# Performance work log

Measured on AMD Instinct MI355X. Metric: run time of the kernel, lower is better.

## Reference

```python
import jax, jax.numpy as jnp
import numpy as np

B, N, NFEAT, NHID, NOUT = 16, 2048, 128, 128, 64
BN_EPS = 1e-5
LRELU_ALPHA = 0.2


def setup_inputs() -> dict:
    key = jax.random.key(0)
    ks = jax.random.split(key, 6)
    stdv = 1.0 / np.sqrt(NHID)
    return {
        "x": jax.random.normal(ks[0], (B, N, NFEAT), dtype=jnp.float32),
        "adj": jnp.zeros((N, N), dtype=jnp.float32),  # passed to GAT but unused
        "adj_gcn": jax.random.uniform(ks[1], (N, N), dtype=jnp.float32),
        "gcn_weight": jax.random.uniform(ks[2], (NFEAT, NHID), minval=-stdv, maxval=stdv, dtype=jnp.float32),
        "gcn_bias": jax.random.uniform(ks[3], (NHID,), minval=-stdv, maxval=stdv, dtype=jnp.float32),
        "bn_gamma": jnp.ones((NHID,), dtype=jnp.float32),
        "bn_beta": jnp.zeros((NHID,), dtype=jnp.float32),
        "gat_W": jax.random.normal(ks[4], (NFEAT, NOUT), dtype=jnp.float32) * 0.05,
    }


def reference(x, adj, adj_gcn, gcn_weight, gcn_bias, bn_gamma, bn_beta, gat_W):
    # --- GCN layer: adj @ (x @ W) + b ---
    support = jnp.einsum("bnc,cd->bnd", x, gcn_weight)
    h = jnp.einsum("nm,bmd->bnd", adj_gcn, support) + gcn_bias  # [B,N,nhid]
    # --- BatchNorm1d (training mode: batch stats over B,N per channel) ---
    mean = h.mean(axis=(0, 1))
    var = h.var(axis=(0, 1))
    h = (h - mean) * jax.lax.rsqrt(var + BN_EPS) * bn_gamma + bn_beta
    # --- ReLU ---
    h = jax.nn.relu(h)
    # --- GAT layer (adj arg unused, as in original) ---
    h_prime = jnp.einsum("bnd,de->bne", h, gat_W)  # [B,N,nout]
    e = jnp.einsum("bne,bme->bnm", h_prime, h_prime)  # [B,N,N]
    e = jnp.where(e > 0, e, LRELU_ALPHA * e)  # LeakyReLU(0.2)
    attention = jax.nn.softmax(e, axis=1)  # softmax over dim=1 (as in source)
    # repeat-mul-sum over dim=2 reduces exactly to row-sum scaling of h_prime
    out = h_prime * attention.sum(axis=2, keepdims=True)  # [B,N,nout]
    return out
```

## Files before the change

### kernel.cpp

```cpp
#include <hip/hip_runtime.h>
#include <math.h>

#define NB 16
#define NN 2048
#define NF 128
#define NH 128
#define NO 64

typedef short bf16x8 __attribute__((ext_vector_type(8)));
typedef float f32x4 __attribute__((ext_vector_type(4)));
typedef unsigned short u16;
typedef unsigned int u32;

#define LOG2E 1.4426950408889634f
#define EXPSHIFT 43.28085122666891f

__device__ __forceinline__ u16 f2bf(float f) {
  u32 u = __builtin_bit_cast(u32, f);
  return (u16)((u + 0x7fffu + ((u >> 16) & 1u)) >> 16);
}
__device__ __forceinline__ float bf2f(u16 h) {
  u32 u = ((u32)h) << 16;
  return __builtin_bit_cast(float, u);
}

__device__ __forceinline__ void gload16(const void* g, void* l) {
  __builtin_amdgcn_global_load_lds((const __attribute__((address_space(1))) void*)g,
                                   (__attribute__((address_space(3))) void*)l, 16, 0, 0);
}
__device__ __forceinline__ f32x4 mfma16(bf16x8 a, bf16x8 b, f32x4 c) {
  return __builtin_amdgcn_mfma_f32_16x16x32_bf16(a, b, c, 0, 0, 0);
}
__device__ __forceinline__ float explr(float z) {
  return __builtin_amdgcn_exp2f(fmaf(fmaxf(z, 0.2f * z), LOG2E, -EXPSHIFT));
}

__global__ __launch_bounds__(256) void k_prep(const float* __restrict__ x,
                                              const float* __restrict__ adj,
                                              const float* __restrict__ gcn_w,
                                              const float* __restrict__ gat_w,
                                              u16* __restrict__ suppT_sw,
                                              u16* __restrict__ adj_sw,
                                              u16* __restrict__ Wg_sw) {
  __shared__ __align__(16) u16 ts[64 * 136];
  __shared__ __align__(16) u16 Bs[16384];
  const int t = threadIdx.x;
  const int bid = blockIdx.x;
  if (bid == 0) {
#pragma unroll
    for (int it = 0; it < 4; ++it) {
      const int s = t + it * 256;
      const int kb = s >> 6, col = s & 63;
      u16 tmp[8];
#pragma unroll
      for (int j = 0; j < 8; ++j) tmp[j] = f2bf(gat_w[(kb * 8 + j) * 64 + col]);
      uint4 o;
      o.x = (u32)tmp[0] | ((u32)tmp[1] << 16);
      o.y = (u32)tmp[2] | ((u32)tmp[3] << 16);
      o.z = (u32)tmp[4] | ((u32)tmp[5] << 16);
      o.w = (u32)tmp[6] | ((u32)tmp[7] << 16);
      *(uint4*)&Wg_sw[(size_t)s * 8] = o;
    }
  } else if (bid < 1025) {
    const int tile = bid - 1;
    const int n0 = (tile >> 5) * 64, m0 = (tile & 31) * 64;
#pragma unroll
    for (int k = 0; k < 4; ++k) {
      const int s = t + k * 256;
      const int row = s >> 4, c4 = (s & 15) * 4;
      const float4 f = *(const float4*)&adj[(size_t)(n0 + row) * 2048 + m0 + c4];
      uint2 pk;
      pk.x = (u32)f2bf(f.x) | ((u32)f2bf(f.y) << 16);
      pk.y = (u32)f2bf(f.z) | ((u32)f2bf(f.w) << 16);
      *(uint2*)&ts[row * 136 + c4] = pk;
    }
    __syncthreads();
#pragma unroll
    for (int k = 0; k < 2; ++k) {
      const int s = t + k * 256;
      const int kb = s >> 6, row = s & 63;
      const uint4 v = *(const uint4*)&ts[row * 136 + kb * 8];
      *(uint4*)&adj_sw[(size_t)tile * 4096 + (size_t)s * 8] = v;
    }
  } else {
    const int sb = bid - 1025;
    const int m0g = sb * 64;
    const int w = t >> 6, l = t & 63;
    const int lg = l >> 4, lr = l & 15;
#pragma unroll
    for (int i = 0; i < 8; ++i) {
      const int s = t + i * 256;
      const int kb = s >> 7, d = s & 127;
      u16 tmp[8];
#pragma unroll
      for (int j = 0; j < 8; ++j) tmp[j] = f2bf(gcn_w[(kb * 8 + j) * 128 + d]);
      uint4 o;
      o.x = (u32)tmp[0] | ((u32)tmp[1] << 16);
      o.y = (u32)tmp[2] | ((u32)tmp[3] << 16);
      o.z = (u32)tmp[4] | ((u32)tmp[5] << 16);
      o.w = (u32)tmp[6] | ((u32)tmp[7] << 16);
      *(uint4*)&Bs[(size_t)s * 8] = o;
    }
#pragma unroll
    for (int k = 0; k < 8; ++k) {
      const int s = t + k * 256;
      const int row = s >> 5, c4 = (s & 31) * 4;
      const float4 f = *(const float4*)&x[(size_t)(m0g + row) * 128 + c4];
      uint2 pk;
      pk.x = (u32)f2bf(f.x) | ((u32)f2bf(f.y) << 16);
      pk.y = (u32)f2bf(f.z) | ((u32)f2bf(f.w) << 16);
      *(uint2*)&ts[row * 136 + c4] = pk;
    }
    __syncthreads();
    f32x4 acc[8];
#pragma unroll
    for (int nf = 0; nf < 8; ++nf) {
      acc[nf][0] = 0.f; acc[nf][1] = 0.f;
      acc[nf][2] = 0.f; acc[nf][3] = 0.f;
    }
#pragma unroll
    for (int ks = 0; ks < 4; ++ks) {
      const int kb = ks * 4 + lg;
      const bf16x8 a = *(const bf16x8*)&ts[(w * 16 + lr) * 136 + kb * 8];
#pragma unroll
      for (int nf = 0; nf < 8; ++nf) {
        const bf16x8 bb = *(const bf16x8*)&Bs[((size_t)kb * 128 + nf * 16 + lr) * 8];
        acc[nf] = mfma16(a, bb, acc[nf]);
      }
    }
    __syncthreads();
    u16* os = Bs;
#pragma unroll
    for (int nf = 0; nf < 8; ++nf) {
      const int d = nf * 16 + lr;
      const int mb = w * 16 + lg * 4;
      const u32 p0 = (u32)f2bf(acc[nf][0]) | ((u32)f2bf(acc[nf][1]) << 16);
      const u32 p1 = (u32)f2bf(acc[nf][2]) | ((u32)f2bf(acc[nf][3]) << 16);
      *(u32*)&os[d * 72 + mb] = p0;
      *(u32*)&os[d * 72 + mb + 2] = p1;
    }
    __syncthreads();
    const int b = m0g >> 11, mt = (m0g & 2047) >> 6;
#pragma unroll
    for (int i = 0; i < 4; ++i) {
      const int s = i * 256 + t;
      const int kb = s >> 7, d = s & 127;
      const uint4 v = *(const uint4*)&os[d * 72 + kb * 8];
      *(uint4*)&suppT_sw[((size_t)((b * 32 + mt) * 8 + kb)) * 1024 + (size_t)d * 8] = v;
    }
  }
}

__global__ __launch_bounds__(512) void k_gcn(const u16* __restrict__ adj_sw,
                                             const u16* __restrict__ suppT_sw,
                                             const float* __restrict__ bias,
                                             float* __restrict__ h,
                                             float* __restrict__ psum,
                                             float* __restrict__ psq) {
  const int flat = blockIdx.y * 32 + blockIdx.x;
  const int nf2 = (flat & 7) * 64 + (flat >> 3);
  const int b = nf2 >> 5, nt = nf2 & 31;
  const int n0 = nt * 64;
  const int t = threadIdx.x;
  const int w = t >> 6, l = t & 63;
  const int wm = w >> 1, wn = w & 1;
  const int lg = l >> 4, lr = l & 15;
  __shared__ __align__(16) u16 As[2][4096];
  __shared__ __align__(16) u16 Bs[2][8192];
  __shared__ float redS[4][128], redQ[4][128];

  f32x4 acc[4];
#pragma unroll
  for (int nf = 0; nf < 4; ++nf) {
    acc[nf][0] = 0.f; acc[nf][1] = 0.f;
    acc[nf][2] = 0.f; acc[nf][3] = 0.f;
  }

#define GCN_STAGE(buf, kt)                                                        \
  {                                                                               \
    gload16(adj_sw + ((size_t)(nt * 32 + (kt))) * 4096 + (size_t)t * 8,           \
            &As[buf][t * 8]);                                                     \
    _Pragma("unroll") for (int i = 0; i < 2; ++i) {                               \
      const int s = i * 512 + t;                                                  \
      gload16(suppT_sw + ((size_t)(b * 32 + (kt))) * 8192 + (size_t)s * 8,        \
              &Bs[buf][s * 8]);                                                   \
    }                                                                             \
  }

  GCN_STAGE(0, 0);
  __syncthreads();
  for (int kt = 0; kt < 32; ++kt) {
    const int cur = kt & 1;
    if (kt + 1 < 32) GCN_STAGE(cur ^ 1, kt + 1);
#pragma unroll
    for (int kb = 0; kb < 2; ++kb) {
      const int ko = kb * 4 + lg;
      const bf16x8 a0 = *(const bf16x8*)&As[cur][(ko * 64 + wm * 16 + lr) * 8];
      const bf16x8 b0 = *(const bf16x8*)&Bs[cur][(ko * 128 + wn * 64 + lr) * 8];
      const bf16x8 b1 = *(const bf16x8*)&Bs[cur][(ko * 128 + wn * 64 + 16 + lr) * 8];
      const bf16x8 b2 = *(const bf16x8*)&Bs[cur][(ko * 128 + wn * 64 + 32 + lr) * 8];
      const bf16x8 b3 = *(const bf16x8*)&Bs[cur][(ko * 128 + wn * 64 + 48 + lr) * 8];
      acc[0] = mfma16(a0, b0, acc[0]);
      acc[1] = mfma16(a0, b1, acc[1]);
      acc[2] = mfma16(a0, b2, acc[2]);
      acc[3] = mfma16(a0, b3, acc[3]);
    }
    __syncthreads();
  }
#undef GCN_STAGE
#pragma unroll
  for (int nf = 0; nf < 4; ++nf) {
    const int d = wn * 64 + nf * 16 + lr;
    const float bv = bias[d];
    float s = 0.f, q = 0.f;
#pragma unroll
    for (int r = 0; r < 4; ++r) {
      const float v = acc[nf][r] + bv;
      const int row = n0 + wm * 16 + lg * 4 + r;
      h[((size_t)(b * NN + row)) * NH + d] = v;
      s += v;
      q = fmaf(v, v, q);
    }
    s += __shfl_xor(s, 16);
    s += __shfl_xor(s, 32);
    q += __shfl_xor(q, 16);
    q += __shfl_xor(q, 32);
    if (lg == 0) {
      redS[wm][d] = s;
      redQ[wm][d] = q;
    }
  }
  __syncthreads();
  if (t < 128) {
    const int blk = b * 32 + nt;
    psum[blk * 128 + t] = redS[0][t] + redS[1][t] + redS[2][t] + redS[3][t];
    psq[blk * 128 + t] = redQ[0][t] + redQ[1][t] + redQ[2][t] + redQ[3][t];
  }
}

__global__ __launch_bounds__(1024) void k_bnstat2(const float* __restrict__ psum,
                                                  const float* __restrict__ psq,
                                                  const float* __restrict__ gamma,
                                                  const float* __restrict__ beta,
                                                  float* __restrict__ scale,
                                                  float* __restrict__ shift) {
  const int t = threadIdx.x;
  const int d = t & 127;
  const int g = t >> 7;
  float s = 0.f, q = 0.f;
  for (int i = g; i < 512; i += 8) {
    s += psum[i * 128 + d];
    q += psq[i * 128 + d];
  }
  __shared__ float ls[8][128], lq[8][128];
  ls[g][d] = s;
  lq[g][d] = q;
  __syncthreads();
  if (t < 128) {
    s = 0.f;
    q = 0.f;
#pragma unroll
    for (int i = 0; i < 8; ++i) {
      s += ls[i][t];
      q += lq[i][t];
    }
    const float inv = 1.f / (float)(NB * NN);
    const float mean = s * inv;
    const float var = q * inv - mean * mean;
    const float sc = gamma[t] * rsqrtf(var + 1e-5f);
    scale[t] = sc;
    shift[t] = beta[t] - mean * sc;
  }
}

__global__ __launch_bounds__(256) void k_hp(const float* __restrict__ h,
                                            const float* __restrict__ scale,
                                            const float* __restrict__ shift,
                                            const u16* __restrict__ Wg_sw,
                                            u16* __restrict__ hp_sw) {
  const int row0 = blockIdx.x * 64;
  const int t = threadIdx.x, w = t >> 6, l = t & 63;
  const int lg = l >> 4, lr = l & 15;
  __shared__ __align__(16) u16 him[8192];
  __shared__ __align__(16) u16 Wg[8192];
  __shared__ __align__(16) u16 hos[64][72];
  __shared__ float scs[128], shs[128];
#pragma unroll
  for (int i = 0; i < 4; ++i) {
    const int s0 = i * 256 + w * 64;
    gload16(Wg_sw + (size_t)(s0 + l) * 8, &Wg[(size_t)s0 * 8]);
  }
  if (t < 128) {
    scs[t] = scale[t];
    shs[t] = shift[t];
  }
  __syncthreads();
#pragma unroll
  for (int k = 0; k < 4; ++k) {
    const int s = t + k * 256;
    const int row = s >> 4, kb = s & 15;
    const float4 v0 = *(const float4*)&h[(size_t)(row0 + row) * NH + kb * 8];
    const float4 v1 = *(const float4*)&h[(size_t)(row0 + row) * NH + kb * 8 + 4];
    u16 p[8];
    p[0] = f2bf(fmaxf(fmaf(v0.x, scs[kb * 8 + 0], shs[kb * 8 + 0]), 0.f));
    p[1] = f2bf(fmaxf(fmaf(v0.y, scs[kb * 8 + 1], shs[kb * 8 + 1]), 0.f));
    p[2] = f2bf(fmaxf(fmaf(v0.z, scs[kb * 8 + 2], shs[kb * 8 + 2]), 0.f));
    p[3] = f2bf(fmaxf(fmaf(v0.w, scs[kb * 8 + 3], shs[kb * 8 + 3]), 0.f));
    p[4] = f2bf(fmaxf(fmaf(v1.x, scs[kb * 8 + 4], shs[kb * 8 + 4]), 0.f));
    p[5] = f2bf(fmaxf(fmaf(v1.y, scs[kb * 8 + 5], shs[kb * 8 + 5]), 0.f));
    p[6] = f2bf(fmaxf(fmaf(v1.z, scs[kb * 8 + 6], shs[kb * 8 + 6]), 0.f));
    p[7] = f2bf(fmaxf(fmaf(v1.w, scs[kb * 8 + 7], shs[kb * 8 + 7]), 0.f));
    uint4 o;
    o.x = (u32)p[0] | ((u32)p[1] << 16);
    o.y = (u32)p[2] | ((u32)p[3] << 16);
    o.z = (u32)p[4] | ((u32)p[5] << 16);
    o.w = (u32)p[6] | ((u32)p[7] << 16);
    const int boff = (row * 256 + kb * 16) ^ ((row & 7) << 4);
    *(uint4*)&him[boff >> 1] = o;
  }
  __syncthreads();
  f32x4 acc[4];
#pragma unroll
  for (int nf = 0; nf < 4; ++nf) {
    acc[nf][0] = 0.f; acc[nf][1] = 0.f;
    acc[nf][2] = 0.f; acc[nf][3] = 0.f;
  }
#pragma unroll
  for (int kks = 0; kks < 4; ++kks) {
    const int ko = kks * 4 + lg;
    const int arow = w * 16 + lr;
    const int aoff = (arow * 256 + ko * 16) ^ ((arow & 7) << 4);
    const bf16x8 a = *(const bf16x8*)&him[aoff >> 1];
#pragma unroll
    for (int nf = 0; nf < 4; ++nf) {
      const bf16x8 bfr = *(const bf16x8*)&Wg[(ko * 64 + nf * 16 + lr) * 8];
      acc[nf] = mfma16(a, bfr, acc[nf]);
    }
  }
#pragma unroll
  for (int nf = 0; nf < 4; ++nf) {
    const int col = nf * 16 + lr;
#pragma unroll
    for (int r = 0; r < 4; ++r) {
      hos[w * 16 + lg * 4 + r][col] = f2bf(acc[nf][r]);
    }
  }
  __syncthreads();
  const size_t tbase = (size_t)blockIdx.x * 4096;
#pragma unroll
  for (int k = 0; k < 2; ++k) {
    const int s = t + k * 256;
    const int kb = s >> 6, r6 = s & 63;
    const uint2 lo = *(const uint2*)&hos[r6][kb * 8];
    const uint2 hi = *(const uint2*)&hos[r6][kb * 8 + 4];
    uint4 o;
    o.x = lo.x; o.y = lo.y; o.z = hi.x; o.w = hi.y;
    *(uint4*)&hp_sw[tbase + kb * 512 + r6 * 8] = o;
  }
}

__global__ __launch_bounds__(256) void k_attnA(const u16* __restrict__ hp_sw,
                                               float* __restrict__ Dpart) {
  const int flat = blockIdx.y * 512 + blockIdx.x;
  const int lf = (flat & 7) * 256 + (flat >> 3);
  const int b = lf >> 7;
  const int qtr = (lf & 127) >> 5;
  const int nt = lf & 31;
  const int t = threadIdx.x, w = t >> 6, l = t & 63;
  const int lg = l >> 4, lr = l & 15;
  const u16* rbase = hp_sw + (size_t)(b * 32 + nt) * 4096;
  const int qrow = (w << 4) + lr;
  const bf16x8 bq0 = *(const bf16x8*)&rbase[(lg * 64 + qrow) * 8];
  const bf16x8 bq1 = *(const bf16x8*)&rbase[((lg + 4) * 64 + qrow) * 8];
  const u16* cb = hp_sw + (size_t)(b * 32 + qtr * 8) * 4096;
  float S = 0.f;
#pragma unroll 2
  for (int mt = 0; mt < 8; ++mt) {
    const u16* base = cb + (size_t)mt * 4096;
#pragma unroll
    for (int mf = 0; mf < 4; ++mf) {
      const bf16x8 a0 = *(const bf16x8*)&base[(lg * 64 + mf * 16 + lr) * 8];
      const bf16x8 a1 = *(const bf16x8*)&base[((lg + 4) * 64 + mf * 16 + lr) * 8];
      f32x4 z;
      z[0] = 0.f; z[1] = 0.f; z[2] = 0.f; z[3] = 0.f;
      __builtin_amdgcn_s_setprio(1);
      z = mfma16(a0, bq0, z);
      z = mfma16(a1, bq1, z);
      __builtin_amdgcn_s_setprio(0);
      S += explr(z[0]) + explr(z[1]) + explr(z[2]) + explr(z[3]);
    }
  }
  S += __shfl_xor(S, 16);
  S += __shfl_xor(S, 32);
  if (l < 16) Dpart[qtr * 32768 + b * NN + nt * 64 + qrow] = S;
}

__global__ __launch_bounds__(512) void k_attnB(const u16* __restrict__ hp_sw,
                                               const float* __restrict__ Dpart,
                                               float* __restrict__ out) {
  const int flat = blockIdx.x;
  const int lf = (flat & 7) * 64 + (flat >> 3);
  const int b = lf >> 5, nt = lf & 31;
  const int t = threadIdx.x, w = t >> 6, l = t & 63;
  const int lg = l >> 4, lr = l & 15;
  const int wr = w & 3;
  const int wh = w >> 2;
  __shared__ float iDs[2048];
  __shared__ float Sv[2][64];
  const u16* rbase = hp_sw + (size_t)(b * 32 + nt) * 4096;
  const int qrow = (wr << 4) + lr;
  const bf16x8 bq0 = *(const bf16x8*)&rbase[(lg * 64 + qrow) * 8];
  const bf16x8 bq1 = *(const bf16x8*)&rbase[((lg + 4) * 64 + qrow) * 8];
#pragma unroll
  for (int i = 0; i < 4; ++i) {
    const int idx = t + i * 512;
    const int n = b * NN + idx;
    iDs[idx] = 1.f / (Dpart[n] + Dpart[32768 + n] + Dpart[65536 + n] + Dpart[98304 + n]);
  }
  __syncthreads();
  const u16* cb = hp_sw + (size_t)(b * 32 + wh * 16) * 4096;
  float S = 0.f;
#pragma unroll 2
  for (int mt = 0; mt < 16; ++mt) {
    const u16* base = cb + (size_t)mt * 4096;
#pragma unroll
    for (int mf = 0; mf < 4; ++mf) {
      const bf16x8 a0 = *(const bf16x8*)&base[(lg * 64 + mf * 16 + lr) * 8];
      const bf16x8 a1 = *(const bf16x8*)&base[((lg + 4) * 64 + mf * 16 + lr) * 8];
      f32x4 z;
      z[0] = 0.f; z[1] = 0.f; z[2] = 0.f; z[3] = 0.f;
      __builtin_amdgcn_s_setprio(1);
      z = mfma16(a0, bq0, z);
      z = mfma16(a1, bq1, z);
      __builtin_amdgcn_s_setprio(0);
      const float4 dv = *(const float4*)&iDs[wh * 1024 + mt * 64 + mf * 16 + lg * 4];
      S = fmaf(explr(z[0]), dv.x, S);
      S = fmaf(explr(z[1]), dv.y, S);
      S = fmaf(explr(z[2]), dv.z, S);
      S = fmaf(explr(z[3]), dv.w, S);
    }
  }
  S += __shfl_xor(S, 16);
  S += __shfl_xor(S, 32);
  if (l < 16) Sv[wh][qrow] = S;
  __syncthreads();
  const int row = t >> 3;
  const int kb = t & 7;
  const float sc = Sv[0][row] + Sv[1][row];
  const size_t R = (size_t)b * NN + nt * 64 + row;
  const uint4 v = *(const uint4*)&rbase[(kb * 64 + row) * 8];
  float4 o0, o1;
  o0.x = bf2f((u16)(v.x & 0xffff)) * sc;
  o0.y = bf2f((u16)(v.x >> 16)) * sc;
  o0.z = bf2f((u16)(v.y & 0xffff)) * sc;
  o0.w = bf2f((u16)(v.y >> 16)) * sc;
  o1.x = bf2f((u16)(v.z & 0xffff)) * sc;
  o1.y = bf2f((u16)(v.z >> 16)) * sc;
  o1.z = bf2f((u16)(v.w & 0xffff)) * sc;
  o1.w = bf2f((u16)(v.w >> 16)) * sc;
  *(float4*)&out[R * NO + kb * 8] = o0;
  *(float4*)&out[R * NO + kb * 8 + 4] = o1;
}

extern "C" void kernel_launch(void* const* d_in, const int* in_sizes, int n_in,
                              void* d_out, int out_size, void* d_ws, size_t ws_size,
                              hipStream_t stream) {
  const float* x = (const float*)d_in[0];
  const float* adj_gcn = (const float*)d_in[2];
  const float* gcn_w = (const float*)d_in[3];
  const float* gcn_b = (const float*)d_in[4];
  const float* gamma = (const float*)d_in[5];
  const float* beta = (const float*)d_in[6];
  const float* gat_w = (const float*)d_in[7];
  float* out = (float*)d_out;
  float* ws = (float*)d_ws;

  u16* adj_sw = (u16*)ws;
  u16* suppT_sw = (u16*)(ws + 2097152);
  float* hbuf = ws + 4194304;
  u16* hp_sw = (u16*)(ws + 8388608);
  float* psum = ws + 9437184;
  float* psq = psum + 65536;
  float* scale = psq + 65536;
  float* shift = scale + 128;
  u16* Wg_sw = (u16*)(shift + 128);
  float* Dpart = ws + 9617664;

  k_prep<<<dim3(1537), dim3(256), 0, stream>>>(x, adj_gcn, gcn_w, gat_w, suppT_sw, adj_sw, Wg_sw);
  k_gcn<<<dim3(32, 16), dim3(512), 0, stream>>>(adj_sw, suppT_sw, gcn_b, hbuf, psum, psq);
  k_bnstat2<<<dim3(1), dim3(1024), 0, stream>>>(psum, psq, gamma, beta, scale, shift);
  k_hp<<<dim3(512), dim3(256), 0, stream>>>(hbuf, scale, shift, Wg_sw, hp_sw);
  k_attnA<<<dim3(512, 4), dim3(256), 0, stream>>>(hp_sw, Dpart);
  k_attnB<<<dim3(512), dim3(512), 0, stream>>>(hp_sw, Dpart, out);
}
```

Before: 107.2 us.

## Double GCN row tile to 128 rows per block for B-tile reuse

The GCN aggregation kernel now computes 128 output rows per block instead of 64. Each warp issues two MFMA row fragments that share the same B-fragment loads, so the support tile is reloaded half as often. The grid shrinks from 512 to 256 blocks, and the partial BN statistics buffers and reduction loop are resized to match. The cost is more LDS and more accumulator registers per block, and 256 blocks may leave some of the GPU's CUs with little work.

```diff
diff --git a/kernel.cpp b/kernel.cpp
--- a/kernel.cpp
+++ b/kernel.cpp
@@ -157,69 +157,86 @@
                                              float* __restrict__ h,
                                              float* __restrict__ psum,
                                              float* __restrict__ psq) {
-  const int flat = blockIdx.y * 32 + blockIdx.x;
-  const int nf2 = (flat & 7) * 64 + (flat >> 3);
-  const int b = nf2 >> 5, nt = nf2 & 31;
-  const int n0 = nt * 64;
+  const int flat = blockIdx.x;
+  const int lf = (flat & 7) * 32 + (flat >> 3);
+  const int b = lf >> 4, ntp = lf & 15;
   const int t = threadIdx.x;
   const int w = t >> 6, l = t & 63;
   const int wm = w >> 1, wn = w & 1;
   const int lg = l >> 4, lr = l & 15;
-  __shared__ __align__(16) u16 As[2][4096];
+  __shared__ __align__(16) u16 As[2][8192];
   __shared__ __align__(16) u16 Bs[2][8192];
   __shared__ float redS[4][128], redQ[4][128];
 
-  f32x4 acc[4];
-#pragma unroll
-  for (int nf = 0; nf < 4; ++nf) {
-    acc[nf][0] = 0.f; acc[nf][1] = 0.f;
-    acc[nf][2] = 0.f; acc[nf][3] = 0.f;
-  }
-
-#define GCN_STAGE(buf, kt)                                                        \
-  {                                                                               \
-    gload16(adj_sw + ((size_t)(nt * 32 + (kt))) * 4096 + (size_t)t * 8,           \
-            &As[buf][t * 8]);                                                     \
-    _Pragma("unroll") for (int i = 0; i < 2; ++i) {                               \
-      const int s = i * 512 + t;                                                  \
-      gload16(suppT_sw + ((size_t)(b * 32 + (kt))) * 8192 + (size_t)s * 8,        \
-              &Bs[buf][s * 8]);                                                   \
-    }                                                                             \
+  f32x4 acc[2][4];
+#pragma unroll
+  for (int mf = 0; mf < 2; ++mf)
+#pragma unroll
+    for (int nf = 0; nf < 4; ++nf) {
+      acc[mf][nf][0] = 0.f; acc[mf][nf][1] = 0.f;
+      acc[mf][nf][2] = 0.f; acc[mf][nf][3] = 0.f;
+    }
+
+#define GCN_STAGE(buf, kt)                                                          \
+  {                                                                                 \
+    _Pragma("unroll") for (int i = 0; i < 2; ++i) {                                 \
+      const int s = i * 512 + t;                            \
+      const int half = s >> 9, inner = s & 511;                                     \
+      gload16(adj_sw + ((size_t)((ntp * 2 + half) * 32 + (kt))) * 4096 +            \
+                  (size_t)inner * 8,                                                \
+              &As[buf][s * 8]);                                                     \
+    }                                                                               \
+    _Pragma("unroll") for (int i = 0; i < 2; ++i) {                                 \
+      const int s = i * 512 + t;                                                    \
+      gload16(suppT_sw + ((size_t)(b * 32 + (kt))) * 8192 + (size_t)s * 8,          \
+              &Bs[buf][s * 8]);                                                     \
+    }                                                                               \
   }
 
   GCN_STAGE(0, 0);
   __syncthreads();
+  const int half = wm >> 1;
   for (int kt = 0; kt < 32; ++kt) {
     const int cur = kt & 1;
     if (kt + 1 < 32) GCN_STAGE(cur ^ 1, kt + 1);
 #pragma unroll
     for (int kb = 0; kb < 2; ++kb) {
       const int ko = kb * 4 + lg;
-      const bf16x8 a0 = *(const bf16x8*)&As[cur][(ko * 64 + wm * 16 + lr) * 8];
+      const int r0 = (wm & 1) * 32 + lr;
+      const bf16x8 a0 = *(const bf16x8*)&As[cur][half * 4096 + (ko * 64 + r0) * 8];
+      const bf16x8 a1 = *(const bf16x8*)&As[cur][half * 4096 + (ko * 64 + r0 + 16) * 8];
       const bf16x8 b0 = *(const bf16x8*)&Bs[cur][(ko * 128 + wn * 64 + lr) * 8];
       const bf16x8 b1 = *(const bf16x8*)&Bs[cur][(ko * 128 + wn * 64 + 16 + lr) * 8];
       const bf16x8 b2 = *(const bf16x8*)&Bs[cur][(ko * 128 + wn * 64 + 32 + lr) * 8];
       const bf16x8 b3 = *(const bf16x8*)&Bs[cur][(ko * 128 + wn * 64 + 48 + lr) * 8];
-      acc[0] = mfma16(a0, b0, acc[0]);
-      acc[1] = mfma16(a0, b1, acc[1]);
-      acc[2] = mfma16(a0, b2, acc[2]);
-      acc[3] = mfma16(a0, b3, acc[3]);
+      acc[0][0] = mfma16(a0, b0, acc[0][0]);
+      acc[0][1] = mfma16(a0, b1, acc[0][1]);
+      acc[0][2] = mfma16(a0, b2, acc[0][2]);
+      acc[0][3] = mfma16(a0, b3, acc[0][3]);
+      acc[1][0] = mfma16(a1, b0, acc[1][0]);
+      acc[1][1] = mfma16(a1, b1, acc[1][1]);
+      acc[1][2] = mfma16(a1, b2, acc[1][2]);
+      acc[1][3] = mfma16(a1, b3, acc[1][3]);
     }
     __syncthreads();
   }
 #undef GCN_STAGE
+  const int n0 = ntp * 128;
 #pragma unroll
   for (int nf = 0; nf < 4; ++nf) {
     const int d = wn * 64 + nf * 16 + lr;
     const float bv = bias[d];
     float s = 0.f, q = 0.f;
 #pragma unroll
-    for (int r = 0; r < 4; ++r) {
-      const float v = acc[nf][r] + bv;
-      const int row = n0 + wm * 16 + lg * 4 + r;
-      h[((size_t)(b * NN + row)) * NH + d] = v;
-      s += v;
-      q = fmaf(v, v, q);
+    for (int mf = 0; mf < 2; ++mf) {
+#pragma unroll
+      for (int r = 0; r < 4; ++r) {
+        const float v = acc[mf][nf][r] + bv;
+        const int row = n0 + wm * 32 + mf * 16 + lg * 4 + r;
+        h[((size_t)(b * NN + row)) * NH + d] = v;
+        s += v;
+        q = fmaf(v, v, q);
+      }
     }
     s += __shfl_xor(s, 16);
     s += __shfl_xor(s, 32);
@@ -232,7 +249,7 @@
   }
   __syncthreads();
   if (t < 128) {
-    const int blk = b * 32 + nt;
+    const int blk = b * 16 + ntp;
     psum[blk * 128 + t] = redS[0][t] + redS[1][t] + redS[2][t] + redS[3][t];
     psq[blk * 128 + t] = redQ[0][t] + redQ[1][t] + redQ[2][t] + redQ[3][t];
   }
@@ -248,7 +265,7 @@
   const int d = t & 127;
   const int g = t >> 7;
   float s = 0.f, q = 0.f;
-  for (int i = g; i < 512; i += 8) {
+  for (int i = g; i < 256; i += 8) {
     s += psum[i * 128 + d];
     q += psq[i * 128 + d];
   }
@@ -480,14 +497,14 @@
   float* hbuf = ws + 4194304;
   u16* hp_sw = (u16*)(ws + 8388608);
   float* psum = ws + 9437184;
-  float* psq = psum + 65536;
-  float* scale = psq + 65536;
+  float* psq = psum + 32768;
+  float* scale = psq + 32768;
   float* shift = scale + 128;
   u16* Wg_sw = (u16*)(shift + 128);
   float* Dpart = ws + 9617664;
 
   k_prep<<<dim3(1537), dim3(256), 0, stream>>>(x, adj_gcn, gcn_w, gat_w, suppT_sw, adj_sw, Wg_sw);
-  k_gcn<<<dim3(32, 16), dim3(512), 0, stream>>>(adj_sw, suppT_sw, gcn_b, hbuf, psum, psq);
+  k_gcn<<<dim3(256), dim3(512), 0, stream>>>(adj_sw, suppT_sw, gcn_b, hbuf, psum, psq);
   k_bnstat2<<<dim3(1), dim3(1024), 0, stream>>>(psum, psq, gamma, beta, scale, shift);
   k_hp<<<dim3(512), dim3(256), 0, stream>>>(hbuf, scale, shift, Wg_sw, hp_sw);
   k_attnA<<<dim3(512, 4), dim3(256), 0, stream>>>(hp_sw, Dpart);
```

Measured after the change: 100.7 us. -6.1%, faster.
